# Kernel optimization log

Hardware: AMD Instinct MI355X
Metric: run time of the kernel (lower is better)

## Reference

```python
import jax, jax.numpy as jnp
import numpy as np

EPS = 1e-15
PROJ_EPS = 4e-3  # standard Poincare-ball projection epsilon (float32)


def _logmap0(x, c):
    sqrt_c = jnp.sqrt(c)
    norm = jnp.maximum(jnp.linalg.norm(x, axis=-1, keepdims=True), EPS)
    arg = jnp.clip(sqrt_c * norm, -1.0 + EPS, 1.0 - EPS)
    return x / (sqrt_c * norm) * jnp.arctanh(arg)


def _expmap0(u, c):
    sqrt_c = jnp.sqrt(c)
    norm = jnp.maximum(jnp.linalg.norm(u, axis=-1, keepdims=True), EPS)
    return jnp.tanh(sqrt_c * norm) * u / (sqrt_c * norm)


def _proj(x, c):
    maxnorm = (1.0 - PROJ_EPS) / jnp.sqrt(c)
    norm = jnp.maximum(jnp.linalg.norm(x, axis=-1, keepdims=True), EPS)
    return jnp.where(norm > maxnorm, x * (maxnorm / norm), x)


def setup_inputs() -> dict:
    key = jax.random.key(0)
    k1, k2, k3, k4 = jax.random.split(key, 4)
    N, E, F = 50000, 800000, 96
    # points strictly inside the Poincare ball
    x = 0.01 * jax.random.normal(k1, (N, F), dtype=jnp.float32)
    edge_index = jax.random.randint(k2, (2, E), 0, N, dtype=jnp.int64)
    W_up = jax.random.normal(k3, (F, F), dtype=jnp.float32) * (1.0 / np.sqrt(F))
    W_lw = jax.random.normal(k4, (1, 2 * F), dtype=jnp.float32) * (1.0 / np.sqrt(2 * F))
    return {"x": x, "edge_index": edge_index, "W_up": W_up, "W_lw": W_lw}


def reference(x, edge_index, W_up, W_lw):
    c = 1.0
    N = x.shape[0]
    row, col = edge_index[0], edge_index[1]  # source j -> target i

    x_tan = _logmap0(x, c)

    # NodeInformationScore: out = (I - D^{-1/2} A D^{-1/2}) x_tan
    ew = jnp.ones(row.shape[0], dtype=x.dtype)
    deg = jax.ops.segment_sum(ew, row, num_segments=N)
    dinv = jnp.where(deg > 0, deg, 1.0) ** -0.5
    dinv = jnp.where(deg > 0, dinv, 0.0)
    norm_e = -dinv[row] * ew * dinv[col]  # edge coefficients; self-loop coeff = 1
    info = jax.ops.segment_sum(norm_e[:, None] * x_tan[row], col, num_segments=N) + x_tan
    score = jnp.sum(jnp.abs(info), axis=1)  # [N]

    updated = jax.nn.leaky_relu(x_tan @ W_up.T, 0.01)  # [N, F]
    sum_neigh = jax.ops.segment_sum(updated[row], col, num_segments=N)

    sel = (score > 1.0).astype(x.dtype)[:, None]  # hot_prob / SEL_v
    sum_sel = jax.ops.segment_sum((sel * updated)[row], col, num_segments=N)

    w_sel = jax.nn.sigmoid(jnp.concatenate([sum_sel, sum_neigh], axis=-1) @ W_lw.T)  # [N,1]
    A_x = jax.nn.relu(jax.ops.segment_sum((w_sel * sel * updated)[row], col, num_segments=N))

    out = updated + A_x
    return _proj(_expmap0(out, c), c)
```

## Files before the change

### kernel.cpp

```cpp
#include <hip/hip_runtime.h>
#include <math.h>

#define FDIM 96
#define CAP 64
#define CAPB 5120
#define EB 8192
#define BLCAP 2048
#define T2MAX 512

typedef float f4 __attribute__((ext_vector_type(4)));
typedef unsigned u32x3 __attribute__((ext_vector_type(3)));

static __device__ __forceinline__ float wave_sum(float v) {
    for (int off = 32; off; off >>= 1) v += __shfl_xor(v, off, 64);
    return v;
}
static __device__ __forceinline__ float half_sum(float v) {
    for (int off = 16; off; off >>= 1) v += __shfl_xor(v, off, 64);
    return v;
}
static __device__ __forceinline__ float grp_sum(float v) {
    v += __shfl_xor(v, 1, 64);
    v += __shfl_xor(v, 2, 64);
    v += __shfl_xor(v, 4, 64);
    return v;
}
static __device__ __forceinline__ float bf_lo(unsigned u) { return __uint_as_float(u << 16); }
static __device__ __forceinline__ float bf_hi(unsigned u) { return __uint_as_float(u & 0xffff0000u); }
static __device__ __forceinline__ unsigned bf_rne(float f) {
    unsigned x = __float_as_uint(f);
    return (x + 0x7fffu + ((x >> 16) & 1u)) >> 16;
}
static __device__ __forceinline__ unsigned f_to_f8(float f) {
    union { _Float16 h; unsigned short u; } c;
    c.h = (_Float16)f;
    unsigned b = (unsigned)c.u + 0x80u;
    return (b >> 8) & 0xffu;
}
static __device__ __forceinline__ float f8h(unsigned hb) {
    union { unsigned short u; _Float16 h; } c;
    c.u = (unsigned short)hb;
    return (float)c.h;
}
static __device__ __forceinline__ float dot4(f4 a) {
    return a.x * a.x + a.y * a.y + a.z * a.z + a.w * a.w;
}

__global__ __launch_bounds__(512) void k_bucket_gemm(
    const int* __restrict__ row, const int* __restrict__ col,
    const float* __restrict__ x, const float* __restrict__ W,
    unsigned* __restrict__ stageC, unsigned char* __restrict__ stageR,
    int* __restrict__ fillC, int* __restrict__ fillR,
    unsigned char* __restrict__ xfb8, unsigned* __restrict__ upb,
    int n, int E, int Gbkt, int t2)
{
    __shared__ __align__(16) char shmem[FDIM * 100 * 4 + 64 * FDIM * 2];
    int t = threadIdx.x;

    if ((int)blockIdx.x < Gbkt) {
        unsigned* stC = (unsigned*)shmem;
        unsigned char* stR = (unsigned char*)(shmem + EB * 4);
        int* histC = (int*)(shmem + EB * 5);
        int* histR = histC + 256;
        int* baseC = histR + 256;
        int* baseR = baseC + 256;
        int* gbC   = baseR + 256;
        int* gbR   = gbC + 256;
        if (t < 256) { histC[t] = 0; histR[t] = 0; }
        __syncthreads();
        int e0 = (int)blockIdx.x * EB;
        unsigned pk[16];
#pragma unroll
        for (int u = 0; u < 16; ++u) {
            int e = e0 + t + u * 512;
            if (e < E) {
                unsigned c = (unsigned)col[e], r = (unsigned)row[e];
                pk[u] = (c << 16) | r;
                atomicAdd(&histC[c >> 8], 1);
                atomicAdd(&histR[r >> 8], 1);
            } else pk[u] = 0xffffffffu;
        }
        __syncthreads();
        if (t < 256) { baseC[t] = histC[t]; baseR[t] = histR[t]; }
        __syncthreads();
        for (int ofs = 1; ofs < 256; ofs <<= 1) {
            int vc = 0, vr = 0;
            if (t < 256 && t >= ofs) { vc = baseC[t - ofs]; vr = baseR[t - ofs]; }
            __syncthreads();
            if (t < 256 && t >= ofs) { baseC[t] += vc; baseR[t] += vr; }
            __syncthreads();
        }
        if (t < 256) {
            baseC[t] -= histC[t];  baseR[t] -= histR[t];
            gbC[t] = histC[t] ? atomicAdd(&fillC[t], histC[t]) : 0;
            gbR[t] = histR[t] ? atomicAdd(&fillR[t], histR[t]) : 0;
        }
        __syncthreads();
#pragma unroll
        for (int u = 0; u < 16; ++u) {
            if (pk[u] != 0xffffffffu) {
                int bc = pk[u] >> 24;
                int br = (pk[u] >> 8) & 0xff;
                int p  = atomicAdd(&baseC[bc], 1);
                stC[p] = pk[u];
                int p2 = atomicAdd(&baseR[br], 1);
                stR[p2] = (unsigned char)(pk[u] & 0xffu);
            }
        }
        __syncthreads();
        int wv = t >> 6, ln = t & 63;
        for (int b = wv; b < 256; b += 8) {
            int lenC = histC[b];
            if (lenC) {
                int s0 = baseC[b] - lenC;
                int room = CAPB - gbC[b]; if (room < 0) room = 0;
                int lim = lenC < room ? lenC : room;
                unsigned* g = stageC + (size_t)b * CAPB + gbC[b];
                for (int k = ln; k < lim; k += 64) g[k] = stC[s0 + k];
            }
            int lenR = histR[b];
            if (lenR) {
                int s1 = baseR[b] - lenR;
                int room = CAPB - gbR[b]; if (room < 0) room = 0;
                int lim = lenR < room ? lenR : room;
                unsigned char* g = stageR + (size_t)b * CAPB + gbR[b];
                for (int k = ln; k < lim; k += 64) g[k] = stR[s1 + k];
            }
        }
        return;
    }

    float* Wsf = (float*)shmem;
    unsigned short* xsb = (unsigned short*)(shmem + FDIM * 100 * 4);
    unsigned* xsb32 = (unsigned*)xsb;
    for (int idx = t; idx < FDIM * FDIM; idx += 512)
        Wsf[(idx / FDIM) * 100 + (idx % FDIM)] = W[idx];
    __syncthreads();
    int tiles = (n + 63) / 64;
    int r0 = t >> 5, c = t & 31;
    for (int tile = (int)blockIdx.x - Gbkt; tile < tiles; tile += t2) {
        int row0 = tile * 64;
#pragma unroll
        for (int rr = 0; rr < 4; ++rr) {
            int lr = r0 + rr * 16;
            int gr = row0 + lr;
            float v0 = 0.f, v1 = 0.f, v2 = 0.f;
            if (gr < n) {
                const float* xr = x + (size_t)gr * FDIM;
                v0 = xr[c]; v1 = xr[c + 32]; v2 = xr[c + 64];
            }
            float ss = half_sum(v0 * v0 + v1 * v1 + v2 * v2);
            float norm = fmaxf(sqrtf(ss), 1e-15f);
            float s = atanhf(fminf(norm, 1.0f)) / norm;
            xsb[lr * FDIM + c]      = (unsigned short)bf_rne(v0 * s);
            xsb[lr * FDIM + c + 32] = (unsigned short)bf_rne(v1 * s);
            xsb[lr * FDIM + c + 64] = (unsigned short)bf_rne(v2 * s);
        }
        __syncthreads();
        for (int idx = t; idx < 64 * 24; idx += 512) {
            int r2 = idx / 24, wq = idx % 24, g = row0 + r2;
            if (g < n) {
                unsigned p0 = xsb32[r2 * 48 + wq * 2];
                unsigned p1 = xsb32[r2 * 48 + wq * 2 + 1];
                unsigned o = f_to_f8(bf_lo(p0)) | (f_to_f8(bf_hi(p0)) << 8)
                           | (f_to_f8(bf_lo(p1)) << 16) | (f_to_f8(bf_hi(p1)) << 24);
                ((unsigned*)xfb8)[(size_t)g * 24 + wq] = o;
            }
        }
        float acc[4][3];
#pragma unroll
        for (int rr = 0; rr < 4; ++rr) { acc[rr][0] = 0.f; acc[rr][1] = 0.f; acc[rr][2] = 0.f; }
#pragma unroll 6
        for (int q = 0; q < 24; ++q) {
            f4 w0 = *(const f4*)&Wsf[c * 100 + q * 4];
            f4 w1 = *(const f4*)&Wsf[(c + 32) * 100 + q * 4];
            f4 w2 = *(const f4*)&Wsf[(c + 64) * 100 + q * 4];
#pragma unroll
            for (int rr = 0; rr < 4; ++rr) {
                uint2 xv = *(const uint2*)&xsb32[(r0 + rr * 16) * 48 + q * 2];
                float x0 = bf_lo(xv.x), x1 = bf_hi(xv.x);
                float x2 = bf_lo(xv.y), x3 = bf_hi(xv.y);
                acc[rr][0] = fmaf(x0, w0.x, fmaf(x1, w0.y, fmaf(x2, w0.z, fmaf(x3, w0.w, acc[rr][0]))));
                acc[rr][1] = fmaf(x0, w1.x, fmaf(x1, w1.y, fmaf(x2, w1.z, fmaf(x3, w1.w, acc[rr][1]))));
                acc[rr][2] = fmaf(x0, w2.x, fmaf(x1, w2.y, fmaf(x2, w2.z, fmaf(x3, w2.w, acc[rr][2]))));
            }
        }
        __syncthreads();
#pragma unroll
        for (int rr = 0; rr < 4; ++rr) {
            int lr = r0 + rr * 16;
            float a0 = acc[rr][0], a1 = acc[rr][1], a2 = acc[rr][2];
            a0 = a0 > 0.f ? a0 : 0.01f * a0;
            a1 = a1 > 0.f ? a1 : 0.01f * a1;
            a2 = a2 > 0.f ? a2 : 0.01f * a2;
            xsb[lr * FDIM + c]      = (unsigned short)bf_rne(a0);
            xsb[lr * FDIM + c + 32] = (unsigned short)bf_rne(a1);
            xsb[lr * FDIM + c + 64] = (unsigned short)bf_rne(a2);
        }
        __syncthreads();
        for (int idx = t; idx < 64 * 48; idx += 512) {
            int r2 = idx / 48, cc = idx % 48, g = row0 + r2;
            if (g < n) upb[(size_t)g * 48 + cc] = xsb32[r2 * 48 + cc];
        }
        __syncthreads();
    }
}

__global__ __launch_bounds__(512) void k_csr_deg(
    const unsigned* __restrict__ stageC, const unsigned char* __restrict__ stageR,
    const int* __restrict__ fillC, const int* __restrict__ fillR,
    float* __restrict__ dinv, int* __restrict__ cnt, unsigned short* __restrict__ srcp,
    int n, int nbuck)
{
    __shared__ __align__(16) char shmem[1024 + 256 * CAP * 2];
    int t = threadIdx.x;
    int bid = (int)blockIdx.x;

    if (bid < nbuck) {
        int* hist = (int*)shmem;
        unsigned short* comp = (unsigned short*)(shmem + 1024);
        if (t < 256) hist[t] = 0;
        __syncthreads();
        int nb = fillC[bid]; if (nb > CAPB) nb = CAPB;
        const unsigned* sc = stageC + (size_t)bid * CAPB;
        for (int k = t; k < nb; k += 512) {
            unsigned pk = sc[k];
            int cl = (pk >> 16) & 255;
            int slot = atomicAdd(&hist[cl], 1);
            if (slot < CAP) comp[cl * CAP + slot] = (unsigned short)(pk & 0xffffu);
        }
        __syncthreads();
        int node0 = bid << 8;
        if (t < 256 && node0 + t < n) cnt[node0 + t] = hist[t];
        int nnode = n - node0; if (nnode > 256) nnode = 256;
        if (nnode > 0) {
            int lim32 = nnode * (CAP / 2);
            unsigned* dst = (unsigned*)(srcp + (size_t)node0 * CAP);
            const unsigned* src = (const unsigned*)comp;
            for (int k = t; k < lim32; k += 512) dst[k] = src[k];
        }
        return;
    }
    int b = bid - nbuck;
    int* hist = (int*)shmem;
    if (t < 256) hist[t] = 0;
    __syncthreads();
    int nb = fillR[b]; if (nb > CAPB) nb = CAPB;
    const unsigned char* sr = stageR + (size_t)b * CAPB;
    for (int k = t; k < nb; k += 512) atomicAdd(&hist[sr[k]], 1);
    __syncthreads();
    int node0 = b << 8;
    if (t < 256 && node0 + t < n) {
        int d = hist[t];
        dinv[node0 + t] = d > 0 ? (float)(1.0 / sqrt((double)d)) : 0.f;
    }
}

#define DEC4(w, cf, A, B, C, D)                              \
    A = fmaf(cf, f8h(((w) & 0xffu) << 8), A);                \
    B = fmaf(cf, f8h((w) & 0xff00u), B);                     \
    C = fmaf(cf, f8h(((w) >> 8) & 0xff00u), C);              \
    D = fmaf(cf, f8h(((w) >> 16) & 0xff00u), D);

__global__ __launch_bounds__(256) void k_pass1(
    const float* __restrict__ x, const unsigned char* __restrict__ xfb8,
    const unsigned short* __restrict__ srcp, const int* __restrict__ cnt,
    const float* __restrict__ dinv, float* __restrict__ sel,
    int* __restrict__ blist, int* __restrict__ nbl, int n)
{
    int t = threadIdx.x;
    int lane = t & 63;
    int gid = lane >> 3, gl = lane & 7;
    int grp = lane & 56;
    int node = (int)blockIdx.x * 32 + (t >> 6) * 8 + gid;
    int nd = node < n ? node : 0;
    int m = cnt[nd];
    if (m > CAP) m = CAP;
    if (node >= n) m = 0;
    float di = dinv[nd];
    int jreg[8]; float cfreg[8];
#pragma unroll
    for (int s = 0; s < 8; ++s) {
        int k = s * 8 + gl;
        int j = (k < m) ? (int)srcp[(size_t)nd * CAP + k] : 0;
        jreg[s] = j;
        cfreg[s] = (k < m) ? -di * dinv[j] : 0.f;
    }
    const f4* xr = (const f4*)(x + (size_t)nd * FDIM + gl * 12);
    f4 o0 = xr[0], o1 = xr[1], o2 = xr[2];
    float ns = grp_sum(dot4(o0) + dot4(o1) + dot4(o2));
    float no = fmaxf(sqrtf(ns), 1e-15f);
    float so = atanhf(fminf(no, 1.0f)) / no;
    float a0 = o0.x*so, a1 = o0.y*so, a2 = o0.z*so, a3 = o0.w*so;
    float a4 = o1.x*so, a5 = o1.y*so, a6 = o1.z*so, a7 = o1.w*so;
    float a8 = o2.x*so, a9 = o2.y*so, a10 = o2.z*so, a11 = o2.w*so;

#pragma unroll
    for (int s = 0; s < 8; ++s) {
        if (s * 8 >= m) break;
        int jv = jreg[s]; float cfv = cfreg[s];
        u32x3 w[8]; float cf[8];
#pragma unroll
        for (int u = 0; u < 8; ++u) {
            int j = __shfl(jv, grp + u, 64);
            cf[u] = __shfl(cfv, grp + u, 64);
            w[u] = *(const u32x3*)(xfb8 + (size_t)j * 96 + gl * 12);
        }
#pragma unroll
        for (int u = 0; u < 8; ++u) {
            DEC4(w[u].x, cf[u], a0, a1, a2, a3)
            DEC4(w[u].y, cf[u], a4, a5, a6, a7)
            DEC4(w[u].z, cf[u], a8, a9, a10, a11)
        }
    }
    float sc = ((fabsf(a0) + fabsf(a1)) + (fabsf(a2) + fabsf(a3)))
             + ((fabsf(a4) + fabsf(a5)) + (fabsf(a6) + fabsf(a7)))
             + ((fabsf(a8) + fabsf(a9)) + (fabsf(a10) + fabsf(a11)));
    sc = grp_sum(sc);
    if (node < n && gl == 0) {
        sel[node] = (sc > 1.0f) ? 1.f : 0.f;
        if (sc > 0.97f && sc < 1.03f) {
            int p = atomicAdd(nbl, 1);
            if (p < BLCAP) blist[p] = node;
        }
    }
}

__global__ __launch_bounds__(256) void k_fix(
    const float* __restrict__ x, const unsigned short* __restrict__ srcp,
    const int* __restrict__ cnt, const float* __restrict__ dinv,
    const int* __restrict__ blist, const int* __restrict__ nbl,
    float* __restrict__ sel, int n)
{
    int nb = *nbl; if (nb > BLCAP) nb = BLCAP;
    int lane = threadIdx.x & 63;
    int w = ((int)blockIdx.x * 256 + (int)threadIdx.x) >> 6;
    int nw = (int)gridDim.x * 4;
    for (int idx = w; idx < nb; idx += nw) {
        int wid = blist[idx];
        float di = dinv[wid];
        int m = cnt[wid]; if (m > CAP) m = CAP;
        int jl = 0; float dvl = 0.f;
        if (lane < m) { jl = srcp[(size_t)wid * CAP + lane]; dvl = dinv[jl]; }
        float2 xo = (lane < 48) ? ((const float2*)(x + (size_t)wid * FDIM))[lane]
                                : make_float2(0.f, 0.f);
        float sso = wave_sum(xo.x * xo.x + xo.y * xo.y);
        float no = fmaxf(sqrtf(sso), 1e-15f);
        float so = atanhf(fminf(no, 1.0f)) / no;
        float fx = xo.x * so, fy = xo.y * so;
        for (int k = 0; k < m; ++k) {
            int jj = __shfl(jl, k, 64);
            float cf = -di * __shfl(dvl, k, 64);
            float2 v = (lane < 48) ? ((const float2*)(x + (size_t)jj * FDIM))[lane]
                                   : make_float2(0.f, 0.f);
            float ssj = wave_sum(v.x * v.x + v.y * v.y);
            float nj = fmaxf(sqrtf(ssj), 1e-15f);
            float sj = atanhf(fminf(nj, 1.0f)) / nj;
            fx = fmaf(cf * sj, v.x, fx);
            fy = fmaf(cf * sj, v.y, fy);
        }
        float sc = wave_sum(fabsf(fx) + fabsf(fy));
        if (lane == 0) sel[wid] = (sc > 1.0f) ? 1.f : 0.f;
    }
}

__global__ __launch_bounds__(256) void k_pass2(
    const unsigned* __restrict__ upb, const unsigned short* __restrict__ srcp,
    const int* __restrict__ cnt, const float* __restrict__ sel,
    const float* __restrict__ Wlw, float* __restrict__ wp, int n)
{
    int wid = (blockIdx.x * blockDim.x + threadIdx.x) >> 6;
    int lane = threadIdx.x & 63;
    if (wid >= n) return;
    if (sel[wid] == 0.f) { if (lane == 0) wp[wid] = 0.f; return; }
    int m = cnt[wid]; if (m > CAP) m = CAP;
    int jl = 0; float sl = 0.f;
    if (lane < m) { jl = srcp[(size_t)wid * CAP + lane]; sl = sel[jl]; }
    float snx = 0.f, sny = 0.f, ssx = 0.f, ssy = 0.f;
    for (int k = 0; k < m; ++k) {
        int j = __shfl(jl, k, 64);
        float sj = __shfl(sl, k, 64);
        if (lane < 48) {
            unsigned q = upb[(size_t)j * 48 + lane];
            float vx = bf_lo(q), vy = bf_hi(q);
            snx += vx; sny += vy;
            ssx = fmaf(sj, vx, ssx); ssy = fmaf(sj, vy, ssy);
        }
    }
    float tv = 0.f;
    if (lane < 48) {
        const float2* Wl = (const float2*)Wlw;
        float2 wsv = Wl[lane];
        float2 wnv = Wl[48 + lane];
        tv = ssx * wsv.x + ssy * wsv.y + snx * wnv.x + sny * wnv.y;
    }
    tv = wave_sum(tv);
    if (lane == 0) wp[wid] = 1.f / (1.f + expf(-tv));
}

__global__ __launch_bounds__(256) void k_pass3(
    const unsigned* __restrict__ upb,
    const unsigned short* __restrict__ srcp, const int* __restrict__ cnt,
    const float* __restrict__ wp, float* __restrict__ out, int n)
{
    int wid = (blockIdx.x * blockDim.x + threadIdx.x) >> 6;
    int lane = threadIdx.x & 63;
    if (wid >= n) return;
    int m = cnt[wid]; if (m > CAP) m = CAP;
    int jl = 0; float pl = 0.f;
    if (lane < m) { jl = srcp[(size_t)wid * CAP + lane]; pl = wp[jl]; }
    unsigned long long ball = __ballot(pl != 0.f);
    float ax = 0.f, ay = 0.f;
    while (ball) {
        int b = __ffsll(ball) - 1;
        ball &= ball - 1;
        int j = __shfl(jl, b, 64);
        float p = __shfl(pl, b, 64);
        if (lane < 48) {
            unsigned u = upb[(size_t)j * 48 + lane];
            ax = fmaf(p, bf_lo(u), ax);
            ay = fmaf(p, bf_hi(u), ay);
        }
    }
    ax = fmaxf(ax, 0.f);
    ay = fmaxf(ay, 0.f);
    unsigned qo = (lane < 48) ? upb[(size_t)wid * 48 + lane] : 0u;
    float ox = bf_lo(qo) + ax, oy = bf_hi(qo) + ay;
    float ss = wave_sum(ox * ox + oy * oy);
    float norm = fmaxf(sqrtf(ss), 1e-15f);
    float th = tanhf(norm);
    float s = th / norm;
    const float maxn = 1.0f - 4e-3f;
    if (th > maxn) s = maxn / norm;
    if (lane < 48) {
        float2* o = (float2*)(out + (size_t)wid * FDIM);
        o[lane] = make_float2(s * ox, s * oy);
    }
}

extern "C" void kernel_launch(void* const* d_in, const int* in_sizes, int n_in,
                              void* d_out, int out_size, void* d_ws, size_t ws_size,
                              hipStream_t stream) {
    const float* x   = (const float*)d_in[0];
    const int*  eidx = (const int*)d_in[1];
    const float* Wup = (const float*)d_in[2];
    const float* Wlw = (const float*)d_in[3];
    float* out = (float*)d_out;

    int N = in_sizes[0] / FDIM;
    int E = in_sizes[1] / 2;
    const int* row = eidx;
    const int* col = eidx + E;
    int nbuck = (N + 255) >> 8;

    char* ws = (char*)d_ws;
    size_t off = 0;
    auto alloc = [&](size_t bytes) {
        void* p = ws + off;
        off += (bytes + 255) & ~(size_t)255;
        return p;
    };
    unsigned char*  xfb8   = (unsigned char*)alloc((size_t)N * 96);
    unsigned*       upb    = (unsigned*)alloc((size_t)N * 48 * 4);
    unsigned*       stageC = (unsigned*)alloc((size_t)nbuck * CAPB * 4);
    unsigned char*  stageR = (unsigned char*)alloc((size_t)nbuck * CAPB);
    int*            fillC  = (int*)alloc((size_t)nbuck * 4);
    int*            fillR  = (int*)alloc((size_t)nbuck * 4);
    float*          dinv   = (float*)alloc((size_t)N * 4);
    int*            cnt    = (int*)alloc((size_t)N * 4);
    float*          sel    = (float*)alloc((size_t)N * 4);
    float*          wp     = (float*)alloc((size_t)N * 4);
    int*            blist  = (int*)alloc((size_t)BLCAP * 4);
    int*            nbl    = (int*)alloc(256);
    unsigned short* srcp   = (unsigned short*)alloc((size_t)N * CAP * 2);

    hipMemsetAsync(fillC, 0, (size_t)nbuck * 4, stream);
    hipMemsetAsync(fillR, 0, (size_t)nbuck * 4, stream);
    hipMemsetAsync(nbl, 0, 4, stream);

    int Gbkt  = (E + EB - 1) / EB;
    int tiles = (N + 63) / 64;
    int t2 = tiles < T2MAX ? tiles : T2MAX;
    dim3 blkF(512);
    dim3 blk(256);
    dim3 gridN4((N + 3) / 4);

    k_bucket_gemm<<<dim3(Gbkt + t2), blkF, 0, stream>>>(
        row, col, x, Wup, stageC, stageR, fillC, fillR, xfb8, upb, N, E, Gbkt, t2);
    k_csr_deg<<<dim3(2 * nbuck), blkF, 0, stream>>>(
        stageC, stageR, fillC, fillR, dinv, cnt, srcp, N, nbuck);
    k_pass1<<<dim3((N + 31) / 32), blk, 0, stream>>>(
        x, xfb8, srcp, cnt, dinv, sel, blist, nbl, N);
    k_fix<<<dim3(256), blk, 0, stream>>>(x, srcp, cnt, dinv, blist, nbl, sel, N);
    k_pass2<<<gridN4, blk, 0, stream>>>(upb, srcp, cnt, sel, Wlw, wp, N);
    k_pass3<<<gridN4, blk, 0, stream>>>(upb, srcp, cnt, wp, out, N);
}
```

Measured before the change: 143.1 us.

## Double-buffer neighbor gathers in pass1 and use 8-lane groups per node in pass3

```diff
diff --git a/kernel.cpp b/kernel.cpp
--- a/kernel.cpp
+++ b/kernel.cpp
@@ -6,7 +6,7 @@
 #define CAPB 5120
 #define EB 8192
 #define BLCAP 2048
-#define T2MAX 512
+#define T2MAX 256
 
 typedef float f4 __attribute__((ext_vector_type(4)));
 typedef unsigned u32x3 __attribute__((ext_vector_type(3)));
@@ -262,7 +262,23 @@
     C = fmaf(cf, f8h(((w) >> 8) & 0xff00u), C);              \
     D = fmaf(cf, f8h(((w) >> 16) & 0xff00u), D);
 
-__global__ __launch_bounds__(256) void k_pass1(
+#define LOADBLK(S, WB, CB)                                               \
+    {   int jv_ = jreg[S]; float cv_ = cfreg[S];                         \
+        _Pragma("unroll")                                                \
+        for (int u_ = 0; u_ < 8; ++u_) {                                 \
+            int j_ = __shfl(jv_, grp + u_, 64);                          \
+            CB[u_] = __shfl(cv_, grp + u_, 64);                          \
+            WB[u_] = *(const u32x3*)(xfb8 + (size_t)j_ * 96 + gl * 12);  \
+        } }
+#define DECBLK(WB, CB)                                                   \
+    _Pragma("unroll")                                                    \
+    for (int u_ = 0; u_ < 8; ++u_) {                                     \
+        DEC4(WB[u_].x, CB[u_], a0, a1, a2, a3)                           \
+        DEC4(WB[u_].y, CB[u_], a4, a5, a6, a7)                           \
+        DEC4(WB[u_].z, CB[u_], a8, a9, a10, a11)                         \
+    }
+
+__global__ __launch_bounds__(256, 4) void k_pass1(
     const float* __restrict__ x, const unsigned char* __restrict__ xfb8,
     const unsigned short* __restrict__ srcp, const int* __restrict__ cnt,
     const float* __restrict__ dinv, float* __restrict__ sel,
@@ -295,22 +311,20 @@
     float a4 = o1.x*so, a5 = o1.y*so, a6 = o1.z*so, a7 = o1.w*so;
     float a8 = o2.x*so, a9 = o2.y*so, a10 = o2.z*so, a11 = o2.w*so;
 
-#pragma unroll
-    for (int s = 0; s < 8; ++s) {
-        if (s * 8 >= m) break;
-        int jv = jreg[s]; float cfv = cfreg[s];
-        u32x3 w[8]; float cf[8];
-#pragma unroll
-        for (int u = 0; u < 8; ++u) {
-            int j = __shfl(jv, grp + u, 64);
-            cf[u] = __shfl(cfv, grp + u, 64);
-            w[u] = *(const u32x3*)(xfb8 + (size_t)j * 96 + gl * 12);
-        }
-#pragma unroll
-        for (int u = 0; u < 8; ++u) {
-            DEC4(w[u].x, cf[u], a0, a1, a2, a3)
-            DEC4(w[u].y, cf[u], a4, a5, a6, a7)
-            DEC4(w[u].z, cf[u], a8, a9, a10, a11)
+    if (m > 0) {
+        int nsb = (m + 7) >> 3;
+        u32x3 wA[8], wB[8]; float cA[8], cB[8];
+        LOADBLK(0, wA, cA)
+#pragma unroll
+        for (int s = 0; s < 8; ++s) {
+            if (s >= nsb) break;
+            if (s & 1) {
+                if (s + 1 < nsb) LOADBLK(s + 1, wA, cA)
+                DECBLK(wB, cB)
+            } else {
+                if (s + 1 < nsb) LOADBLK(s + 1, wB, cB)
+                DECBLK(wA, cA)
+            }
         }
     }
     float sc = ((fabsf(a0) + fabsf(a1)) + (fabsf(a2) + fabsf(a3)))
@@ -403,38 +417,70 @@
     const unsigned short* __restrict__ srcp, const int* __restrict__ cnt,
     const float* __restrict__ wp, float* __restrict__ out, int n)
 {
-    int wid = (blockIdx.x * blockDim.x + threadIdx.x) >> 6;
-    int lane = threadIdx.x & 63;
-    if (wid >= n) return;
-    int m = cnt[wid]; if (m > CAP) m = CAP;
-    int jl = 0; float pl = 0.f;
-    if (lane < m) { jl = srcp[(size_t)wid * CAP + lane]; pl = wp[jl]; }
-    unsigned long long ball = __ballot(pl != 0.f);
-    float ax = 0.f, ay = 0.f;
-    while (ball) {
-        int b = __ffsll(ball) - 1;
-        ball &= ball - 1;
-        int j = __shfl(jl, b, 64);
-        float p = __shfl(pl, b, 64);
-        if (lane < 48) {
-            unsigned u = upb[(size_t)j * 48 + lane];
-            ax = fmaf(p, bf_lo(u), ax);
-            ay = fmaf(p, bf_hi(u), ay);
-        }
-    }
-    ax = fmaxf(ax, 0.f);
-    ay = fmaxf(ay, 0.f);
-    unsigned qo = (lane < 48) ? upb[(size_t)wid * 48 + lane] : 0u;
-    float ox = bf_lo(qo) + ax, oy = bf_hi(qo) + ay;
-    float ss = wave_sum(ox * ox + oy * oy);
+    int t = threadIdx.x;
+    int lane = t & 63;
+    int gid = lane >> 3, gl = lane & 7;
+    int grp = lane & 56;
+    int node = (int)blockIdx.x * 32 + (t >> 6) * 8 + gid;
+    int nd = node < n ? node : 0;
+    int m = cnt[nd]; if (m > CAP) m = CAP;
+    if (node >= n) m = 0;
+    float pl[8]; int jl[8];
+#pragma unroll
+    for (int s = 0; s < 8; ++s) {
+        int k = s * 8 + gl;
+        int j = (k < m) ? (int)srcp[(size_t)nd * CAP + k] : 0;
+        jl[s] = j;
+        pl[s] = (k < m) ? wp[j] : 0.f;
+    }
+    float any = 0.f;
+#pragma unroll
+    for (int s = 0; s < 8; ++s) any += pl[s];
+    any = grp_sum(any);
+    float b0=0.f,b1=0.f,b2=0.f,b3=0.f,b4=0.f,b5=0.f,b6=0.f,b7=0.f,b8=0.f,b9=0.f,b10=0.f,b11=0.f;
+    if (any > 0.f) {
+#pragma unroll
+        for (int s = 0; s < 8; ++s) {
+            if (s * 8 >= m) break;
+            float pv = pl[s]; int jv = jl[s];
+            for (int u = 0; u < 8; ++u) {
+                float p = __shfl(pv, grp + u, 64);
+                if (p != 0.f) {
+                    int j = __shfl(jv, grp + u, 64);
+                    const uint2* uj = (const uint2*)(upb + (size_t)j * 48 + gl * 6);
+                    uint2 q0 = uj[0], q1 = uj[1], q2 = uj[2];
+                    b0 = fmaf(p, bf_lo(q0.x), b0); b1 = fmaf(p, bf_hi(q0.x), b1);
+                    b2 = fmaf(p, bf_lo(q0.y), b2); b3 = fmaf(p, bf_hi(q0.y), b3);
+                    b4 = fmaf(p, bf_lo(q1.x), b4); b5 = fmaf(p, bf_hi(q1.x), b5);
+                    b6 = fmaf(p, bf_lo(q1.y), b6); b7 = fmaf(p, bf_hi(q1.y), b7);
+                    b8 = fmaf(p, bf_lo(q2.x), b8); b9 = fmaf(p, bf_hi(q2.x), b9);
+                    b10 = fmaf(p, bf_lo(q2.y), b10); b11 = fmaf(p, bf_hi(q2.y), b11);
+                }
+            }
+        }
+    }
+    b0 = fmaxf(b0, 0.f); b1 = fmaxf(b1, 0.f); b2 = fmaxf(b2, 0.f); b3 = fmaxf(b3, 0.f);
+    b4 = fmaxf(b4, 0.f); b5 = fmaxf(b5, 0.f); b6 = fmaxf(b6, 0.f); b7 = fmaxf(b7, 0.f);
+    b8 = fmaxf(b8, 0.f); b9 = fmaxf(b9, 0.f); b10 = fmaxf(b10, 0.f); b11 = fmaxf(b11, 0.f);
+    const uint2* uo = (const uint2*)(upb + (size_t)nd * 48 + gl * 6);
+    uint2 q0 = uo[0], q1 = uo[1], q2 = uo[2];
+    float o0 = bf_lo(q0.x)+b0, o1 = bf_hi(q0.x)+b1, o2 = bf_lo(q0.y)+b2, o3 = bf_hi(q0.y)+b3;
+    float o4 = bf_lo(q1.x)+b4, o5 = bf_hi(q1.x)+b5, o6 = bf_lo(q1.y)+b6, o7 = bf_hi(q1.y)+b7;
+    float o8 = bf_lo(q2.x)+b8, o9 = bf_hi(q2.x)+b9, o10 = bf_lo(q2.y)+b10, o11 = bf_hi(q2.y)+b11;
+    float ss = grp_sum(((o0*o0+o1*o1)+(o2*o2+o3*o3))+((o4*o4+o5*o5)+(o6*o6+o7*o7))
+                      +((o8*o8+o9*o9)+(o10*o10+o11*o11)));
     float norm = fmaxf(sqrtf(ss), 1e-15f);
     float th = tanhf(norm);
     float s = th / norm;
     const float maxn = 1.0f - 4e-3f;
     if (th > maxn) s = maxn / norm;
-    if (lane < 48) {
-        float2* o = (float2*)(out + (size_t)wid * FDIM);
-        o[lane] = make_float2(s * ox, s * oy);
+    if (node < n) {
+        f4* o = (f4*)(out + (size_t)node * FDIM + gl * 12);
+        f4 w0, w1, w2;
+        w0.x = s*o0; w0.y = s*o1; w0.z = s*o2; w0.w = s*o3;
+        w1.x = s*o4; w1.y = s*o5; w1.z = s*o6; w1.w = s*o7;
+        w2.x = s*o8; w2.y = s*o9; w2.z = s*o10; w2.w = s*o11;
+        o[0] = w0; o[1] = w1; o[2] = w2;
     }
 }
 
@@ -493,5 +539,5 @@
         x, xfb8, srcp, cnt, dinv, sel, blist, nbl, N);
     k_fix<<<dim3(256), blk, 0, stream>>>(x, srcp, cnt, dinv, blist, nbl, sel, N);
     k_pass2<<<gridN4, blk, 0, stream>>>(upb, srcp, cnt, sel, Wlw, wp, N);
-    k_pass3<<<gridN4, blk, 0, stream>>>(upb, srcp, cnt, wp, out, N);
-}
+    k_pass3<<<dim3((N + 31) / 32), blk, 0, stream>>>(upb, srcp, cnt, wp, out, N);
+}
```

After: 175.5 us. 1.23x slower.
